# Optimization experiments

Measured on AMD Instinct MI355X. Metric: run time of the kernel, lower is better.

## Reference

```python
import jax, jax.numpy as jnp
import numpy as np

E = 4
OUT_CH = 32
IN_CH = 32
KSIZE = 3
PAD = 1
TEMPERATURE = 30.0
HIDDEN = IN_CH // 4  # ratio=4


def _dyn_conv(x, w):
    """Per-sample conv. x: [B,C,H,W], w: [B,O,C,k,k] -> [B,O,H,W] (pad=1, stride=1)."""
    def one(xi, wi):
        return jax.lax.conv_general_dilated(
            xi[None], wi, window_strides=(1, 1), padding=[(PAD, PAD), (PAD, PAD)],
            dimension_numbers=('NCHW', 'OIHW', 'NCHW'))[0]
    return jax.vmap(one)(x, w)


def setup_inputs() -> dict:
    key = jax.random.key(0)
    ks = jax.random.split(key, 6)
    x = jax.random.normal(ks[0], (16, IN_CH, 256, 256), dtype=jnp.float32)
    # ControlModule 1x1 convs (bias=False) expressed as matrices
    w_c1 = jax.random.normal(ks[1], (HIDDEN, IN_CH), dtype=jnp.float32) * (2.0 / IN_CH) ** 0.5
    w_c2 = jax.random.normal(ks[2], (E * OUT_CH, HIDDEN), dtype=jnp.float32) * (2.0 / HIDDEN) ** 0.5
    weight1 = jax.random.normal(ks[3], (E, OUT_CH, IN_CH, KSIZE, KSIZE), dtype=jnp.float32)
    weight2 = jax.random.normal(ks[4], (E, OUT_CH, OUT_CH, KSIZE, KSIZE), dtype=jnp.float32)
    weight3 = jax.random.normal(ks[5], (E, OUT_CH, OUT_CH, KSIZE, KSIZE), dtype=jnp.float32)
    return {"x": x, "w_c1": w_c1, "w_c2": w_c2,
            "weight1": weight1, "weight2": weight2, "weight3": weight3}


def reference(x, w_c1, w_c2, weight1, weight2, weight3):
    B = x.shape[0]
    # ControlModule: global average pool -> 1x1 conv -> relu -> 1x1 conv -> softmax over E
    gap = x.mean(axis=(2, 3))                      # [B, C]
    h = jax.nn.relu(gap @ w_c1.T)                  # [B, hidden]
    coeff = (h @ w_c2.T).reshape(B, OUT_CH, E)     # [B, O, E]
    coeff = jax.nn.softmax(coeff / TEMPERATURE, axis=2)

    def assemble(w):  # w: [E, O, C, k, k] -> per-sample [B, O, C, k, k]
        flat = w.reshape(E, OUT_CH, -1)
        agg = jnp.einsum('boe,eoc->boc', coeff, flat)
        return agg.reshape(B, OUT_CH, *w.shape[2:])

    w1 = assemble(weight1)
    w2 = assemble(weight2)
    w3 = assemble(weight3)

    out = _dyn_conv(x, w1)
    out = _dyn_conv(out, w2)
    out = _dyn_conv(out, w3)
    return out
```

## Files before the change

### kernel.cpp

```cpp
#include <hip/hip_runtime.h>

typedef __attribute__((ext_vector_type(8))) short bf16x8;
typedef __attribute__((ext_vector_type(4))) float f32x4;

#define TEMP_ 30.0f
#define MFMA(A,B,C) __builtin_amdgcn_mfma_f32_16x16x32_bf16(A,B,C,0,0,0)

static __device__ inline unsigned short f2bf(float f) {
    unsigned u = __builtin_bit_cast(unsigned, f);
    u = (u + 0x7FFFu + ((u >> 16) & 1u)) >> 16;
    return (unsigned short)u;
}
static __device__ inline unsigned packbf(float a, float b) {
    return (unsigned)f2bf(a) | ((unsigned)f2bf(b) << 16);
}
static __device__ inline bf16x8 bc16(uint4 v) { return __builtin_bit_cast(bf16x8, v); }

__global__ __launch_bounds__(256) void gap_cvt_kernel(
    const float* __restrict__ x, float* __restrict__ gap,
    unsigned short* __restrict__ xbf)
{
    __shared__ unsigned short sm[32 * 4 * 258];
    __shared__ float red[4][32];
    int b = blockIdx.y, ys = blockIdx.x * 4;
    int t = threadIdx.x, wv = t >> 6, ln = t & 63;

    const float* xb = x + (((size_t)b * 32) << 16) + ((size_t)(ys + wv) << 8) + ln * 4;
    float part[32];
#pragma unroll
    for (int c = 0; c < 32; ++c) {
        float4 v = *(const float4*)(xb + ((size_t)c << 16));
        part[c] = v.x + v.y + v.z + v.w;
        unsigned* wp = (unsigned*)&sm[c * 1032 + wv * 258 + ln * 4];
        wp[0] = packbf(v.x, v.y);
        wp[1] = packbf(v.z, v.w);
    }
#pragma unroll
    for (int c = 0; c < 32; ++c) {
#pragma unroll
        for (int off = 32; off; off >>= 1) part[c] += __shfl_xor(part[c], off);
    }
    if (ln == 0) {
#pragma unroll
        for (int c = 0; c < 32; ++c) red[wv][c] = part[c];
    }
    __syncthreads();
    if (t < 32) {
        float s = red[0][t] + red[1][t] + red[2][t] + red[3][t];
        atomicAdd(&gap[b * 32 + t], s * (1.f / 65536.f));
    }
    uint4* outp = (uint4*)xbf;
    int cg = wv;
#pragma unroll
    for (int it = 0; it < 16; ++it) {
        int px = it * 64 + ln;
        int y = px >> 8, xx = px & 255;
        unsigned short h[8];
#pragma unroll
        for (int i = 0; i < 8; ++i) h[i] = sm[(cg * 8 + i) * 1032 + y * 258 + xx];
        uint4 v;
        v.x = (unsigned)h[0] | ((unsigned)h[1] << 16);
        v.y = (unsigned)h[2] | ((unsigned)h[3] << 16);
        v.z = (unsigned)h[4] | ((unsigned)h[5] << 16);
        v.w = (unsigned)h[6] | ((unsigned)h[7] << 16);
        outp[((((size_t)b << 16) + ((size_t)(ys + y) << 8) + xx) << 2) + cg] = v;
    }
}

__global__ __launch_bounds__(256) void assemble_kernel(
    const float* __restrict__ gap,
    const float* __restrict__ w_c1,
    const float* __restrict__ w_c2,
    const float* __restrict__ wt1,
    const float* __restrict__ wt2,
    const float* __restrict__ wt3,
    unsigned short* __restrict__ wo1,
    unsigned short* __restrict__ wo2,
    unsigned short* __restrict__ wo3)
{
    int b = blockIdx.x;
    int sel = blockIdx.y;
    int t = threadIdx.x;
    __shared__ float gap_s[32], h_s[8], logit_s[128], coeff_s[32][4];
    if (t < 32) gap_s[t] = gap[b * 32 + t];
    __syncthreads();
    if (t < 8) {
        float a = 0.f;
        for (int c = 0; c < 32; ++c) a += gap_s[c] * w_c1[t * 32 + c];
        h_s[t] = a > 0.f ? a : 0.f;
    }
    __syncthreads();
    if (t < 128) {
        float a = 0.f;
        for (int k = 0; k < 8; ++k) a += h_s[k] * w_c2[t * 8 + k];
        logit_s[t] = a * (1.0f / TEMP_);
    }
    __syncthreads();
    if (t < 32) {
        float m = -1e30f;
        for (int e = 0; e < 4; ++e) m = fmaxf(m, logit_s[t * 4 + e]);
        float ex[4], sum = 0.f;
        for (int e = 0; e < 4; ++e) { ex[e] = expf(logit_s[t * 4 + e] - m); sum += ex[e]; }
        for (int e = 0; e < 4; ++e) coeff_s[t][e] = ex[e] / sum;
    }
    __syncthreads();

    const float* wt = sel == 0 ? wt1 : (sel == 1 ? wt2 : wt3);
    unsigned short* wo = sel == 0 ? wo1 : (sel == 1 ? wo2 : wo3);

    for (int idx = t; idx < 9216; idx += 256) {
        int d = idx >> 10;
        int o = (idx >> 5) & 31;
        int c = idx & 31;
        int j = c * 9 + d;
        float v = coeff_s[o][0] * wt[(0 * 32 + o) * 288 + j]
                + coeff_s[o][1] * wt[(1 * 32 + o) * 288 + j]
                + coeff_s[o][2] * wt[(2 * 32 + o) * 288 + j]
                + coeff_s[o][3] * wt[(3 * 32 + o) * 288 + j];
        wo[(size_t)b * 9216 + idx] = f2bf(v);
    }
}

__global__ __launch_bounds__(512, 2) void fused_conv3(
    const unsigned short* __restrict__ xbf,
    const unsigned short* __restrict__ w1,
    const unsigned short* __restrict__ w2,
    const unsigned short* __restrict__ w3,
    float* __restrict__ out)
{
    __shared__ uint4 lds[7192];
    int b  = blockIdx.z;
    int x0 = blockIdx.x * 32, y0 = blockIdx.y * 16;
    int t  = threadIdx.x;
    int l15 = t & 15, kg = (t >> 4) & 3, wv = t >> 6;

    const uint4* wp1 = (const uint4*)(w1 + (size_t)b * 9216);
    const uint4* wp2 = (const uint4*)(w2 + (size_t)b * 9216);
    const uint4* wp3 = (const uint4*)(w3 + (size_t)b * 9216);

    bf16x8 wfA[9][2], wfB[9][2];
#pragma unroll
    for (int d = 0; d < 9; ++d) {
        wfA[d][0] = bc16(wp1[(d * 32 + l15) * 4 + kg]);
        wfA[d][1] = bc16(wp1[(d * 32 + 16 + l15) * 4 + kg]);
    }

    const unsigned short* xb = xbf + (((size_t)b) << 16) * 32;
    for (int it = 0; it < 7; ++it) {
        int tau = it * 512 + t;
        if (tau < 3344) {
            int y = tau / 152, rem = tau - y * 152;
            int xx = rem >> 2, cg = rem & 3;
            int gy = y0 - 3 + y, gx = x0 - 3 + xx;
            uint4 v = make_uint4(0u, 0u, 0u, 0u);
            if ((unsigned)gy < 256u && (unsigned)gx < 256u)
                v = *(const uint4*)(xb + ((((size_t)gy << 8) + gx) << 5) + (cg << 3));
            lds[tau] = v;
        }
    }
#pragma unroll
    for (int d = 0; d < 9; ++d) {
        wfB[d][0] = bc16(wp2[(d * 32 + l15) * 4 + kg]);
        wfB[d][1] = bc16(wp2[(d * 32 + 16 + l15) * 4 + kg]);
    }
    __syncthreads();

    const bf16x8* LA = (const bf16x8*)lds;
    const bf16x8* L1 = (const bf16x8*)(lds + 3344);
    unsigned short* SA = (unsigned short*)lds;
    unsigned short* S1 = (unsigned short*)(lds + 3344);

    for (int i = wv; i < 60; i += 8) {
        int row = i / 3, xt = i - row * 3;
        int Xp = xt * 16 + l15;
        int base = (row * 38 + Xp) * 4 + kg;
        f32x4 a0 = {0.f,0.f,0.f,0.f}, a1 = {0.f,0.f,0.f,0.f};
#pragma unroll
        for (int d = 0; d < 9; ++d) {
            bf16x8 bfr = LA[base + (d / 3) * 152 + (d % 3) * 4];
            a0 = MFMA(wfA[d][0], bfr, a0);
            a1 = MFMA(wfA[d][1], bfr, a1);
        }
        bool live = ((unsigned)(y0 - 2 + row) < 256u) && ((unsigned)(x0 - 2 + Xp) < 256u);
        uint2 p0, p1;
        p0.x = packbf(a0[0], a0[1]); p0.y = packbf(a0[2], a0[3]);
        p1.x = packbf(a1[0], a1[1]); p1.y = packbf(a1[2], a1[3]);
        if (!live) { p0.x = p0.y = p1.x = p1.y = 0u; }
        unsigned short* dp = S1 + ((row * 48 + Xp) << 5);
        *(uint2*)(dp + (kg << 2))      = p0;
        *(uint2*)(dp + 16 + (kg << 2)) = p1;
    }
#pragma unroll
    for (int d = 0; d < 9; ++d) {
        wfA[d][0] = bc16(wp3[(d * 32 + l15) * 4 + kg]);
        wfA[d][1] = bc16(wp3[(d * 32 + 16 + l15) * 4 + kg]);
    }
    __syncthreads();

    for (int i = wv; i < 54; i += 8) {
        int row = i / 3, xt = i - row * 3;
        int Xp = xt * 16 + l15;
        int base = (row * 48 + Xp) * 4 + kg;
        f32x4 a0 = {0.f,0.f,0.f,0.f}, a1 = {0.f,0.f,0.f,0.f};
#pragma unroll
        for (int d = 0; d < 9; ++d) {
            bf16x8 bfr = L1[base + (d / 3) * 192 + (d % 3) * 4];
            a0 = MFMA(wfB[d][0], bfr, a0);
            a1 = MFMA(wfB[d][1], bfr, a1);
        }
        if (Xp < 34) {
            bool live = ((unsigned)(y0 - 1 + row) < 256u) && ((unsigned)(x0 - 1 + Xp) < 256u);
            uint2 p0, p1;
            p0.x = packbf(a0[0], a0[1]); p0.y = packbf(a0[2], a0[3]);
            p1.x = packbf(a1[0], a1[1]); p1.y = packbf(a1[2], a1[3]);
            if (!live) { p0.x = p0.y = p1.x = p1.y = 0u; }
            unsigned short* dp = SA + ((row * 34 + Xp) << 5);
            *(uint2*)(dp + (kg << 2))      = p0;
            *(uint2*)(dp + 16 + (kg << 2)) = p1;
        }
    }
    __syncthreads();

    for (int i = wv; i < 32; i += 8) {
        int row = i >> 1, xt = i & 1;
        int Xp = xt * 16 + l15;
        int base = (row * 34 + Xp) * 4 + kg;
        f32x4 a0 = {0.f,0.f,0.f,0.f}, a1 = {0.f,0.f,0.f,0.f};
#pragma unroll
        for (int d = 0; d < 9; ++d) {
            bf16x8 bfr = LA[base + (d / 3) * 136 + (d % 3) * 4];
            a0 = MFMA(wfA[d][0], bfr, a0);
            a1 = MFMA(wfA[d][1], bfr, a1);
        }
        int gy = y0 + row, gx = x0 + Xp;
        float* dp = out + (((size_t)b * 32 + kg * 4) << 16) + ((size_t)gy << 8) + gx;
#pragma unroll
        for (int r2 = 0; r2 < 4; ++r2) {
            dp[(size_t)r2 << 16]        = a0[r2];
            dp[(size_t)(r2 + 16) << 16] = a1[r2];
        }
    }
}

extern "C" void kernel_launch(void* const* d_in, const int* in_sizes, int n_in,
                              void* d_out, int out_size, void* d_ws, size_t ws_size,
                              hipStream_t stream) {
    const float* x    = (const float*)d_in[0];
    const float* w_c1 = (const float*)d_in[1];
    const float* w_c2 = (const float*)d_in[2];
    const float* wt1  = (const float*)d_in[3];
    const float* wt2  = (const float*)d_in[4];
    const float* wt3  = (const float*)d_in[5];
    float* out = (float*)d_out;

    char* ws = (char*)d_ws;
    float* gap = (float*)ws;
    unsigned short* w1 = (unsigned short*)(ws + 4096);
    unsigned short* w2 = (unsigned short*)(ws + 4096 + 294912);
    unsigned short* w3 = (unsigned short*)(ws + 4096 + 2 * 294912);
    unsigned short* xbf = (unsigned short*)(ws + 1048576);

    hipMemsetAsync(gap, 0, 2048, stream);
    gap_cvt_kernel<<<dim3(64, 16), 256, 0, stream>>>(x, gap, xbf);
    assemble_kernel<<<dim3(16, 3), 256, 0, stream>>>(gap, w_c1, w_c2,
                                                     wt1, wt2, wt3, w1, w2, w3);
    fused_conv3<<<dim3(8, 16, 16), 512, 0, stream>>>(xbf, w1, w2, w3, out);
}
```

Baseline: 389.1 us.

## Use channel-group planar LDS layout, 1024-thread conv blocks, coalesced bf16 stores

The fused conv kernel now stores activations in LDS as four channel-group planes instead of interleaving them per pixel. Each lane's MFMA B-fragment reads become contiguous across lanes, which should reduce bank conflicts. Block size doubles to 1024 threads (16 waves) with launch bounds of 1024,4, and the halo load is unrolled. The GAP/convert kernel pads its LDS stride and writes xbf with linear coalesced stores. The trade-off is heavier register pressure under the tighter launch bounds, which could cause spills since 36 weight fragments are held in registers.

```diff
diff --git a/kernel.cpp b/kernel.cpp
--- a/kernel.cpp
+++ b/kernel.cpp
@@ -16,11 +16,12 @@
 }
 static __device__ inline bf16x8 bc16(uint4 v) { return __builtin_bit_cast(bf16x8, v); }
 
+#define SM_S 1034
 __global__ __launch_bounds__(256) void gap_cvt_kernel(
     const float* __restrict__ x, float* __restrict__ gap,
     unsigned short* __restrict__ xbf)
 {
-    __shared__ unsigned short sm[32 * 4 * 258];
+    __shared__ unsigned short sm[32 * SM_S];
     __shared__ float red[4][32];
     int b = blockIdx.y, ys = blockIdx.x * 4;
     int t = threadIdx.x, wv = t >> 6, ln = t & 63;
@@ -31,7 +32,7 @@
     for (int c = 0; c < 32; ++c) {
         float4 v = *(const float4*)(xb + ((size_t)c << 16));
         part[c] = v.x + v.y + v.z + v.w;
-        unsigned* wp = (unsigned*)&sm[c * 1032 + wv * 258 + ln * 4];
+        unsigned* wp = (unsigned*)&sm[c * SM_S + wv * 258 + ln * 4];
         wp[0] = packbf(v.x, v.y);
         wp[1] = packbf(v.z, v.w);
     }
@@ -50,20 +51,21 @@
         atomicAdd(&gap[b * 32 + t], s * (1.f / 65536.f));
     }
     uint4* outp = (uint4*)xbf;
-    int cg = wv;
+    size_t base = (((size_t)b << 16) + ((size_t)ys << 8)) << 2;
 #pragma unroll
     for (int it = 0; it < 16; ++it) {
-        int px = it * 64 + ln;
+        int g = it * 256 + t;
+        int cgq = g & 3, px = g >> 2;
         int y = px >> 8, xx = px & 255;
         unsigned short h[8];
 #pragma unroll
-        for (int i = 0; i < 8; ++i) h[i] = sm[(cg * 8 + i) * 1032 + y * 258 + xx];
+        for (int i = 0; i < 8; ++i) h[i] = sm[(cgq * 8 + i) * SM_S + y * 258 + xx];
         uint4 v;
         v.x = (unsigned)h[0] | ((unsigned)h[1] << 16);
         v.y = (unsigned)h[2] | ((unsigned)h[3] << 16);
         v.z = (unsigned)h[4] | ((unsigned)h[5] << 16);
         v.w = (unsigned)h[6] | ((unsigned)h[7] << 16);
-        outp[((((size_t)b << 16) + ((size_t)(ys + y) << 8) + xx) << 2) + cg] = v;
+        outp[base + g] = v;
     }
 }
 
@@ -121,7 +123,7 @@
     }
 }
 
-__global__ __launch_bounds__(512, 2) void fused_conv3(
+__global__ __launch_bounds__(1024, 4) void fused_conv3(
     const unsigned short* __restrict__ xbf,
     const unsigned short* __restrict__ w1,
     const unsigned short* __restrict__ w2,
@@ -146,16 +148,17 @@
     }
 
     const unsigned short* xb = xbf + (((size_t)b) << 16) * 32;
-    for (int it = 0; it < 7; ++it) {
-        int tau = it * 512 + t;
+#pragma unroll
+    for (int it = 0; it < 4; ++it) {
+        int tau = it * 1024 + t;
         if (tau < 3344) {
-            int y = tau / 152, rem = tau - y * 152;
-            int xx = rem >> 2, cg = rem & 3;
+            int px = tau >> 2, cg = tau & 3;
+            int y = px / 38, xx = px - y * 38;
             int gy = y0 - 3 + y, gx = x0 - 3 + xx;
             uint4 v = make_uint4(0u, 0u, 0u, 0u);
             if ((unsigned)gy < 256u && (unsigned)gx < 256u)
                 v = *(const uint4*)(xb + ((((size_t)gy << 8) + gx) << 5) + (cg << 3));
-            lds[tau] = v;
+            lds[cg * 836 + px] = v;
         }
     }
 #pragma unroll
@@ -169,15 +172,16 @@
     const bf16x8* L1 = (const bf16x8*)(lds + 3344);
     unsigned short* SA = (unsigned short*)lds;
     unsigned short* S1 = (unsigned short*)(lds + 3344);
-
-    for (int i = wv; i < 60; i += 8) {
+    int pl0 = kg >> 1, half = (kg & 1) << 2;
+
+    for (int i = wv; i < 60; i += 16) {
         int row = i / 3, xt = i - row * 3;
         int Xp = xt * 16 + l15;
-        int base = (row * 38 + Xp) * 4 + kg;
+        int base = kg * 836 + row * 38 + Xp;
         f32x4 a0 = {0.f,0.f,0.f,0.f}, a1 = {0.f,0.f,0.f,0.f};
 #pragma unroll
         for (int d = 0; d < 9; ++d) {
-            bf16x8 bfr = LA[base + (d / 3) * 152 + (d % 3) * 4];
+            bf16x8 bfr = LA[base + (d / 3) * 38 + (d % 3)];
             a0 = MFMA(wfA[d][0], bfr, a0);
             a1 = MFMA(wfA[d][1], bfr, a1);
         }
@@ -186,9 +190,9 @@
         p0.x = packbf(a0[0], a0[1]); p0.y = packbf(a0[2], a0[3]);
         p1.x = packbf(a1[0], a1[1]); p1.y = packbf(a1[2], a1[3]);
         if (!live) { p0.x = p0.y = p1.x = p1.y = 0u; }
-        unsigned short* dp = S1 + ((row * 48 + Xp) << 5);
-        *(uint2*)(dp + (kg << 2))      = p0;
-        *(uint2*)(dp + 16 + (kg << 2)) = p1;
+        unsigned short* dp = S1 + ((row * 48 + Xp) << 3) + half;
+        *(uint2*)(dp + pl0 * 7680)       = p0;
+        *(uint2*)(dp + (2 + pl0) * 7680) = p1;
     }
 #pragma unroll
     for (int d = 0; d < 9; ++d) {
@@ -197,14 +201,14 @@
     }
     __syncthreads();
 
-    for (int i = wv; i < 54; i += 8) {
+    for (int i = wv; i < 54; i += 16) {
         int row = i / 3, xt = i - row * 3;
         int Xp = xt * 16 + l15;
-        int base = (row * 48 + Xp) * 4 + kg;
+        int base = kg * 960 + row * 48 + Xp;
         f32x4 a0 = {0.f,0.f,0.f,0.f}, a1 = {0.f,0.f,0.f,0.f};
 #pragma unroll
         for (int d = 0; d < 9; ++d) {
-            bf16x8 bfr = L1[base + (d / 3) * 192 + (d % 3) * 4];
+            bf16x8 bfr = L1[base + (d / 3) * 48 + (d % 3)];
             a0 = MFMA(wfB[d][0], bfr, a0);
             a1 = MFMA(wfB[d][1], bfr, a1);
         }
@@ -214,21 +218,21 @@
             p0.x = packbf(a0[0], a0[1]); p0.y = packbf(a0[2], a0[3]);
             p1.x = packbf(a1[0], a1[1]); p1.y = packbf(a1[2], a1[3]);
             if (!live) { p0.x = p0.y = p1.x = p1.y = 0u; }
-            unsigned short* dp = SA + ((row * 34 + Xp) << 5);
-            *(uint2*)(dp + (kg << 2))      = p0;
-            *(uint2*)(dp + 16 + (kg << 2)) = p1;
-        }
-    }
-    __syncthreads();
-
-    for (int i = wv; i < 32; i += 8) {
+            unsigned short* dp = SA + ((row * 34 + Xp) << 3) + half;
+            *(uint2*)(dp + pl0 * 4896)       = p0;
+            *(uint2*)(dp + (2 + pl0) * 4896) = p1;
+        }
+    }
+    __syncthreads();
+
+    for (int i = wv; i < 32; i += 16) {
         int row = i >> 1, xt = i & 1;
         int Xp = xt * 16 + l15;
-        int base = (row * 34 + Xp) * 4 + kg;
+        int base = kg * 612 + row * 34 + Xp;
         f32x4 a0 = {0.f,0.f,0.f,0.f}, a1 = {0.f,0.f,0.f,0.f};
 #pragma unroll
         for (int d = 0; d < 9; ++d) {
-            bf16x8 bfr = LA[base + (d / 3) * 136 + (d % 3) * 4];
+            bf16x8 bfr = LA[base + (d / 3) * 34 + (d % 3)];
             a0 = MFMA(wfA[d][0], bfr, a0);
             a1 = MFMA(wfA[d][1], bfr, a1);
         }
@@ -264,5 +268,5 @@
     gap_cvt_kernel<<<dim3(64, 16), 256, 0, stream>>>(x, gap, xbf);
     assemble_kernel<<<dim3(16, 3), 256, 0, stream>>>(gap, w_c1, w_c2,
                                                      wt1, wt2, wt3, w1, w2, w3);
-    fused_conv3<<<dim3(8, 16, 16), 512, 0, stream>>>(xbf, w1, w2, w3, out);
-}
+    fused_conv3<<<dim3(8, 16, 16), 1024, 0, stream>>>(xbf, w1, w2, w3, out);
+}
```

Result: slower. 609.0 us (+56.5%).
